# Optimization experiments

Hardware: AMD Instinct MI355X
Metric: run time of the kernel (lower is better)

The kernel has to match this reference:

```python
import jax, jax.numpy as jnp
import numpy as np

N_NODES = 50000
N_EDGES = 1250000
D_FEAT = 64


def setup_inputs() -> dict:
    key = jax.random.key(0)
    k1, k2, k3, k4 = jax.random.split(key, 4)
    feat = jax.random.normal(k1, (N_NODES, D_FEAT), dtype=jnp.float32)
    edge_weight = jax.random.uniform(k2, (N_EDGES,), dtype=jnp.float32)
    edge_src = jax.random.randint(k3, (N_EDGES,), 0, N_NODES, dtype=jnp.int64)
    edge_dst = jnp.sort(jax.random.randint(k4, (N_EDGES,), 0, N_NODES, dtype=jnp.int64))
    return {"feat": feat, "edge_weight": edge_weight,
            "edge_src": edge_src, "edge_dst": edge_dst}


def reference(feat, edge_weight, edge_src, edge_dst):
    # u_mul_e: gather source node features, scale by per-edge weight
    msgs = feat[edge_src] * edge_weight[:, None]          # [E, d]
    # fn.sum: scatter-add messages to destination nodes
    rst = jax.ops.segment_sum(msgs, edge_dst, num_segments=N_NODES)  # [N, d]
    return rst
```

## Files before the change

### kernel.cpp

```cpp
#include <hip/hip_runtime.h>

#define D_FEAT 64

__global__ __launch_bounds__(256) void build_rowptr_scatter(
    const int* __restrict__ edge_dst, int* __restrict__ rp,
    int n_edges, int n_nodes) {
  const int e = blockIdx.x * blockDim.x + threadIdx.x;
  if (e > n_edges) return;
  const int d0 = (e == 0) ? -1 : edge_dst[e - 1];
  const int d1 = (e == n_edges) ? n_nodes : edge_dst[e];
  for (int v = d0 + 1; v <= d1; ++v) rp[v] = e;
}

__global__ __launch_bounds__(256) void gcn_gather4(
    const float* __restrict__ feat,
    const float* __restrict__ ew,
    const int* __restrict__ esrc,
    const int* __restrict__ rp,
    float* __restrict__ out, int n_nodes) {
  const int wave = (blockIdx.x * blockDim.x + threadIdx.x) >> 6;
  const int lane = threadIdx.x & 63;
  if (wave >= n_nodes) return;
  const int sub = lane >> 4;
  const int fl  = lane & 15;

  const int e0 = rp[wave];
  const int e1 = rp[wave + 1];

  float4 a0 = {0.f, 0.f, 0.f, 0.f};
  float4 a1 = {0.f, 0.f, 0.f, 0.f};
  float4 a2 = {0.f, 0.f, 0.f, 0.f};
  float4 a3 = {0.f, 0.f, 0.f, 0.f};

  const float4* feat4 = (const float4*)feat;

  for (int base = e0; base < e1; base += 64) {
    const int n = min(64, e1 - base);
    int   s = 0;
    float w = 0.0f;
    if (lane < n) {
      s = esrc[base + lane];
      w = ew[base + lane];
    }
    for (int i = 0; i < n; i += 16) {
      const int   s0 = __shfl(s, i + sub);
      const float w0 = __shfl(w, i + sub);
      const int   s1 = __shfl(s, i + 4 + sub);
      const float w1 = __shfl(w, i + 4 + sub);
      const int   s2 = __shfl(s, i + 8 + sub);
      const float w2 = __shfl(w, i + 8 + sub);
      const int   s3 = __shfl(s, i + 12 + sub);
      const float w3 = __shfl(w, i + 12 + sub);
      const float4 r0 = feat4[(size_t)s0 * 16 + fl];
      const float4 r1 = feat4[(size_t)s1 * 16 + fl];
      const float4 r2 = feat4[(size_t)s2 * 16 + fl];
      const float4 r3 = feat4[(size_t)s3 * 16 + fl];
      a0.x = fmaf(r0.x, w0, a0.x); a0.y = fmaf(r0.y, w0, a0.y);
      a0.z = fmaf(r0.z, w0, a0.z); a0.w = fmaf(r0.w, w0, a0.w);
      a1.x = fmaf(r1.x, w1, a1.x); a1.y = fmaf(r1.y, w1, a1.y);
      a1.z = fmaf(r1.z, w1, a1.z); a1.w = fmaf(r1.w, w1, a1.w);
      a2.x = fmaf(r2.x, w2, a2.x); a2.y = fmaf(r2.y, w2, a2.y);
      a2.z = fmaf(r2.z, w2, a2.z); a2.w = fmaf(r2.w, w2, a2.w);
      a3.x = fmaf(r3.x, w3, a3.x); a3.y = fmaf(r3.y, w3, a3.y);
      a3.z = fmaf(r3.z, w3, a3.z); a3.w = fmaf(r3.w, w3, a3.w);
    }
  }

  float4 acc;
  acc.x = (a0.x + a1.x) + (a2.x + a3.x);
  acc.y = (a0.y + a1.y) + (a2.y + a3.y);
  acc.z = (a0.z + a1.z) + (a2.z + a3.z);
  acc.w = (a0.w + a1.w) + (a2.w + a3.w);

  acc.x += __shfl_xor(acc.x, 16);
  acc.y += __shfl_xor(acc.y, 16);
  acc.z += __shfl_xor(acc.z, 16);
  acc.w += __shfl_xor(acc.w, 16);
  acc.x += __shfl_xor(acc.x, 32);
  acc.y += __shfl_xor(acc.y, 32);
  acc.z += __shfl_xor(acc.z, 32);
  acc.w += __shfl_xor(acc.w, 32);

  if (lane < 16) {
    ((float4*)(out + (size_t)wave * D_FEAT))[fl] = acc;
  }
}

extern "C" void kernel_launch(void* const* d_in, const int* in_sizes, int n_in,
                              void* d_out, int out_size, void* d_ws, size_t ws_size,
                              hipStream_t stream) {
  const float* feat        = (const float*)d_in[0];
  const float* edge_weight = (const float*)d_in[1];
  const int*   edge_src    = (const int*)d_in[2];
  const int*   edge_dst    = (const int*)d_in[3];
  float* out = (float*)d_out;

  const int n_edges = in_sizes[1];
  const int n_nodes = out_size / D_FEAT;

  int* rp = (int*)d_ws;

  const int bp_threads = n_edges + 1;
  build_rowptr_scatter<<<(bp_threads + 255) / 256, 256, 0, stream>>>(
      edge_dst, rp, n_edges, n_nodes);

  const int total_threads = n_nodes * 64;
  gcn_gather4<<<(total_threads + 255) / 256, 256, 0, stream>>>(
      feat, edge_weight, edge_src, rp, out, n_nodes);
}
```

Baseline: 113.2 us.

## Process two destination nodes per wave with weight-split accumulators

Each wavefront now handles two consecutive destination nodes. It walks their combined edge range in one loop and masks each edge's weight into node A or node B accumulators by comparing the edge index with the row boundary. This is meant to cut the tail waste of partly filled 16-edge iterations, since the average degree is about 25 and is not a multiple of 16, and to halve the number of waves. In exchange every edge costs twice the FMAs, and there is half as many waves to hide gather latency.

```diff
diff --git a/kernel.cpp b/kernel.cpp
--- a/kernel.cpp
+++ b/kernel.cpp
@@ -12,7 +12,7 @@
   for (int v = d0 + 1; v <= d1; ++v) rp[v] = e;
 }
 
-__global__ __launch_bounds__(256) void gcn_gather4(
+__global__ __launch_bounds__(256) void gcn_gather4x2(
     const float* __restrict__ feat,
     const float* __restrict__ ew,
     const int* __restrict__ esrc,
@@ -20,22 +20,24 @@
     float* __restrict__ out, int n_nodes) {
   const int wave = (blockIdx.x * blockDim.x + threadIdx.x) >> 6;
   const int lane = threadIdx.x & 63;
-  if (wave >= n_nodes) return;
+  const int vA = wave * 2;
+  if (vA >= n_nodes) return;
+  const bool hasB = (vA + 1) < n_nodes;
+
   const int sub = lane >> 4;
   const int fl  = lane & 15;
 
-  const int e0 = rp[wave];
-  const int e1 = rp[wave + 1];
+  const int r0 = rp[vA];
+  const int r1 = rp[vA + 1];
+  const int r2 = hasB ? rp[vA + 2] : r1;
 
-  float4 a0 = {0.f, 0.f, 0.f, 0.f};
-  float4 a1 = {0.f, 0.f, 0.f, 0.f};
-  float4 a2 = {0.f, 0.f, 0.f, 0.f};
-  float4 a3 = {0.f, 0.f, 0.f, 0.f};
+  float4 aA = {0.f, 0.f, 0.f, 0.f};
+  float4 aB = {0.f, 0.f, 0.f, 0.f};
 
   const float4* feat4 = (const float4*)feat;
 
-  for (int base = e0; base < e1; base += 64) {
-    const int n = min(64, e1 - base);
+  for (int base = r0; base < r2; base += 64) {
+    const int n = min(64, r2 - base);
     int   s = 0;
     float w = 0.0f;
     if (lane < n) {
@@ -51,38 +53,57 @@
       const float w2 = __shfl(w, i + 8 + sub);
       const int   s3 = __shfl(s, i + 12 + sub);
       const float w3 = __shfl(w, i + 12 + sub);
-      const float4 r0 = feat4[(size_t)s0 * 16 + fl];
-      const float4 r1 = feat4[(size_t)s1 * 16 + fl];
-      const float4 r2 = feat4[(size_t)s2 * 16 + fl];
-      const float4 r3 = feat4[(size_t)s3 * 16 + fl];
-      a0.x = fmaf(r0.x, w0, a0.x); a0.y = fmaf(r0.y, w0, a0.y);
-      a0.z = fmaf(r0.z, w0, a0.z); a0.w = fmaf(r0.w, w0, a0.w);
-      a1.x = fmaf(r1.x, w1, a1.x); a1.y = fmaf(r1.y, w1, a1.y);
-      a1.z = fmaf(r1.z, w1, a1.z); a1.w = fmaf(r1.w, w1, a1.w);
-      a2.x = fmaf(r2.x, w2, a2.x); a2.y = fmaf(r2.y, w2, a2.y);
-      a2.z = fmaf(r2.z, w2, a2.z); a2.w = fmaf(r2.w, w2, a2.w);
-      a3.x = fmaf(r3.x, w3, a3.x); a3.y = fmaf(r3.y, w3, a3.y);
-      a3.z = fmaf(r3.z, w3, a3.z); a3.w = fmaf(r3.w, w3, a3.w);
+
+      const float4 q0 = feat4[(size_t)s0 * 16 + fl];
+      const float4 q1 = feat4[(size_t)s1 * 16 + fl];
+      const float4 q2 = feat4[(size_t)s2 * 16 + fl];
+      const float4 q3 = feat4[(size_t)s3 * 16 + fl];
+
+      const int i0 = base + i + sub;
+      const int i1 = i0 + 4;
+      const int i2 = i0 + 8;
+      const int i3 = i0 + 12;
+      const float w0A = (i0 < r1) ? w0 : 0.f; const float w0B = w0 - w0A;
+      const float w1A = (i1 < r1) ? w1 : 0.f; const float w1B = w1 - w1A;
+      const float w2A = (i2 < r1) ? w2 : 0.f; const float w2B = w2 - w2A;
+      const float w3A = (i3 < r1) ? w3 : 0.f; const float w3B = w3 - w3A;
+
+      aA.x = fmaf(q0.x, w0A, aA.x); aA.y = fmaf(q0.y, w0A, aA.y);
+      aA.z = fmaf(q0.z, w0A, aA.z); aA.w = fmaf(q0.w, w0A, aA.w);
+      aB.x = fmaf(q0.x, w0B, aB.x); aB.y = fmaf(q0.y, w0B, aB.y);
+      aB.z = fmaf(q0.z, w0B, aB.z); aB.w = fmaf(q0.w, w0B, aB.w);
+
+      aA.x = fmaf(q1.x, w1A, aA.x); aA.y = fmaf(q1.y, w1A, aA.y);
+      aA.z = fmaf(q1.z, w1A, aA.z); aA.w = fmaf(q1.w, w1A, aA.w);
+      aB.x = fmaf(q1.x, w1B, aB.x); aB.y = fmaf(q1.y, w1B, aB.y);
+      aB.z = fmaf(q1.z, w1B, aB.z); aB.w = fmaf(q1.w, w1B, aB.w);
+
+      aA.x = fmaf(q2.x, w2A, aA.x); aA.y = fmaf(q2.y, w2A, aA.y);
+      aA.z = fmaf(q2.z, w2A, aA.z); aA.w = fmaf(q2.w, w2A, aA.w);
+      aB.x = fmaf(q2.x, w2B, aB.x); aB.y = fmaf(q2.y, w2B, aB.y);
+      aB.z = fmaf(q2.z, w2B, aB.z); aB.w = fmaf(q2.w, w2B, aB.w);
+
+      aA.x = fmaf(q3.x, w3A, aA.x); aA.y = fmaf(q3.y, w3A, aA.y);
+      aA.z = fmaf(q3.z, w3A, aA.z); aA.w = fmaf(q3.w, w3A, aA.w);
+      aB.x = fmaf(q3.x, w3B, aB.x); aB.y = fmaf(q3.y, w3B, aB.y);
+      aB.z = fmaf(q3.z, w3B, aB.z); aB.w = fmaf(q3.w, w3B, aB.w);
     }
   }
 
-  float4 acc;
-  acc.x = (a0.x + a1.x) + (a2.x + a3.x);
-  acc.y = (a0.y + a1.y) + (a2.y + a3.y);
-  acc.z = (a0.z + a1.z) + (a2.z + a3.z);
-  acc.w = (a0.w + a1.w) + (a2.w + a3.w);
+  aA.x += __shfl_xor(aA.x, 16); aA.y += __shfl_xor(aA.y, 16);
+  aA.z += __shfl_xor(aA.z, 16); aA.w += __shfl_xor(aA.w, 16);
+  aA.x += __shfl_xor(aA.x, 32); aA.y += __shfl_xor(aA.y, 32);
+  aA.z += __shfl_xor(aA.z, 32); aA.w += __shfl_xor(aA.w, 32);
 
-  acc.x += __shfl_xor(acc.x, 16);
-  acc.y += __shfl_xor(acc.y, 16);
-  acc.z += __shfl_xor(acc.z, 16);
-  acc.w += __shfl_xor(acc.w, 16);
-  acc.x += __shfl_xor(acc.x, 32);
-  acc.y += __shfl_xor(acc.y, 32);
-  acc.z += __shfl_xor(acc.z, 32);
-  acc.w += __shfl_xor(acc.w, 32);
+  aB.x += __shfl_xor(aB.x, 16); aB.y += __shfl_xor(aB.y, 16);
+  aB.z += __shfl_xor(aB.z, 16); aB.w += __shfl_xor(aB.w, 16);
+  aB.x += __shfl_xor(aB.x, 32); aB.y += __shfl_xor(aB.y, 32);
+  aB.z += __shfl_xor(aB.z, 32); aB.w += __shfl_xor(aB.w, 32);
 
   if (lane < 16) {
-    ((float4*)(out + (size_t)wave * D_FEAT))[fl] = acc;
+    ((float4*)(out + (size_t)vA * D_FEAT))[fl] = aA;
+  } else if (lane < 32 && hasB) {
+    ((float4*)(out + (size_t)(vA + 1) * D_FEAT))[fl] = aB;
   }
 }
 
@@ -104,7 +125,8 @@
   build_rowptr_scatter<<<(bp_threads + 255) / 256, 256, 0, stream>>>(
       edge_dst, rp, n_edges, n_nodes);
 
-  const int total_threads = n_nodes * 64;
-  gcn_gather4<<<(total_threads + 255) / 256, 256, 0, stream>>>(
+  const int n_waves = (n_nodes + 1) / 2;
+  const long total_threads = (long)n_waves * 64;
+  gcn_gather4x2<<<(int)((total_threads + 255) / 256), 256, 0, stream>>>(
       feat, edge_weight, edge_src, rp, out, n_nodes);
 }
```

Result: no change. 113.5 us (+0.3%).
